# Kernel tuning notes

Hardware: AMD Instinct MI355X
Metric: run time of the kernel (lower is better)

## Reference

```python
import jax, jax.numpy as jnp
import numpy as np

HEADS = 8
DIM_HEAD = 32
EPS = 1e-5


def _rel_index(h, w):
    # matches Attention._generate_relative_index (static, computed on host)
    coords = np.stack(np.meshgrid(np.arange(h), np.arange(w), indexing='ij')).reshape(2, -1)
    rel = coords[:, :, None] - coords[:, None, :]  # [2, n, n]
    rel[0] += h - 1
    rel[1] += w - 1
    rel[0] *= 2 * w - 1
    idx = rel.sum(0).reshape(-1)
    # torch.clamp(relative_index, 0, max_index) -- indices are already in range here
    return jnp.asarray(np.clip(idx, 0, (2 * h - 1) * (2 * w - 1) - 1))


def _layernorm(x, g, b):
    m = jnp.mean(x, axis=-1, keepdims=True)
    v = jnp.var(x, axis=-1, keepdims=True)
    return (x - m) * jax.lax.rsqrt(v + EPS) * g + b


def setup_inputs() -> dict:
    key = jax.random.key(0)
    ks = jax.random.split(key, 6)
    B, C, H, W = 64, 384, 16, 16
    inner = HEADS * DIM_HEAD  # 256
    hid = 4 * C               # 1536
    def nrm(k, shape, s=0.02):
        return jax.random.normal(k, shape, jnp.float32) * s
    return {
        'x': jax.random.normal(ks[0], (B, C, H, W), jnp.float32),
        'ln1_g': jnp.ones((C,), jnp.float32),
        'ln1_b': jnp.zeros((C,), jnp.float32),
        'w_qkv': nrm(ks[1], (C, 3 * inner)),
        'bias_table': nrm(ks[2], ((2 * H - 1) * (2 * W - 1), HEADS)),
        'w_out': nrm(ks[3], (inner, C)),
        'b_out': jnp.zeros((C,), jnp.float32),
        'ln2_g': jnp.ones((C,), jnp.float32),
        'ln2_b': jnp.zeros((C,), jnp.float32),
        'w_ff1': nrm(ks[4], (C, hid)),
        'b_ff1': jnp.zeros((hid,), jnp.float32),
        'w_ff2': nrm(ks[5], (hid, C)),
        'b_ff2': jnp.zeros((C,), jnp.float32),
    }


def reference(x, ln1_g, ln1_b, w_qkv, bias_table, w_out, b_out,
              ln2_g, ln2_b, w_ff1, b_ff1, w_ff2, b_ff2):
    B, C, H, W = x.shape
    n = H * W
    t = x.reshape(B, C, n).transpose(0, 2, 1)  # [B, n, C]

    # --- attention branch (PreNorm(LayerNorm) -> Attention) ---
    a = _layernorm(t, ln1_g, ln1_b)
    qkv = a @ w_qkv  # [B, n, 3*inner]
    q, k, v = jnp.split(qkv, 3, axis=-1)
    def split_heads(z):
        return z.reshape(B, n, HEADS, DIM_HEAD).transpose(0, 2, 1, 3)  # [B, h, n, d]
    q, k, v = split_heads(q), split_heads(k), split_heads(v)
    dots = jnp.einsum('bhid,bhjd->bhij', q, k) * (DIM_HEAD ** -0.5)
    idx = _rel_index(H, W)  # [n*n]
    rel_bias = bias_table[idx].reshape(n, n, HEADS).transpose(2, 0, 1)[None]  # [1, h, n, n]
    attn = jax.nn.softmax(dots + rel_bias, axis=-1)
    o = jnp.einsum('bhij,bhjd->bhid', attn, v)
    o = o.transpose(0, 2, 1, 3).reshape(B, n, HEADS * DIM_HEAD)
    attn_out = o @ w_out + b_out  # to_out Linear (dropout=0)

    # --- feedforward branch (PreNorm(LayerNorm) -> FFN) ---
    f = _layernorm(t, ln2_g, ln2_b)
    f = jax.nn.gelu(f @ w_ff1 + b_ff1, approximate=False) @ w_ff2 + b_ff2

    y = t + attn_out + f  # x_adjusted + attn_out + ff_out
    return y.transpose(0, 2, 1).reshape(B, C, H, W)
```

## Files before the change

### kernel.cpp

```cpp
#include <hip/hip_runtime.h>

typedef __bf16 bf16;
typedef __bf16 bf16x8 __attribute__((ext_vector_type(8)));
typedef float f32x4 __attribute__((ext_vector_type(4)));

__device__ __forceinline__ void gll16(const void* g, void* l) {
    __builtin_amdgcn_global_load_lds((const __attribute__((address_space(1))) void*)g,
                                     (__attribute__((address_space(3))) void*)l, 16, 0, 0);
}

__device__ __forceinline__ float gelu_f(float v) {
    float x2 = v * v;
    float sn = v * fmaf(-0.0713540072f, x2, -1.5957691216f);
    float e  = __expf(sn);
    return v * __builtin_amdgcn_rcpf(1.0f + e);
}

__launch_bounds__(256)
__global__ void prep_kernel(const float* __restrict__ wqkv, const float* __restrict__ wout,
                            const float* __restrict__ wff1, const float* __restrict__ wff2,
                            bf16* __restrict__ wqkvT, bf16* __restrict__ woutT,
                            bf16* __restrict__ wff1T, bf16* __restrict__ wff2T,
                            const float* __restrict__ x,
                            const float* __restrict__ g1, const float* __restrict__ b1,
                            const float* __restrict__ g2, const float* __restrict__ b2,
                            bf16* __restrict__ a, bf16* __restrict__ f) {
    __shared__ __align__(16) float smem[12672 + 512 + 64];
    const int tid = threadIdx.x;
    int g = blockIdx.x;
    if (g < 1536) {
        float (*tl)[33] = (float (*)[33])smem;
        const float* in; bf16* out; int R, Cc, bx, by;
        if (g < 288)       { in = wqkv; out = wqkvT; R = 384;  Cc = 768;  bx = g % 24; by = g / 24; }
        else if (g < 384)  { g -= 288; in = wout; out = woutT; R = 256;  Cc = 384;  bx = g % 12; by = g / 12; }
        else if (g < 960)  { g -= 384; in = wff1; out = wff1T; R = 384;  Cc = 1536; bx = g % 48; by = g / 48; }
        else               { g -= 960; in = wff2; out = wff2T; R = 1536; Cc = 384;  bx = g % 12; by = g / 12; }
        const int c0 = bx * 32, r0 = by * 32;
        const int cl = tid & 31, r8 = tid >> 5;
#pragma unroll
        for (int k = 0; k < 4; k++) {
            int r = k * 8 + r8;
            tl[r][cl] = in[(size_t)(r0 + r) * Cc + c0 + cl];
        }
        __syncthreads();
#pragma unroll
        for (int k = 0; k < 4; k++) {
            int cc = k * 8 + r8;
            out[(size_t)(c0 + cc) * R + r0 + cl] = (bf16)tl[cl][cc];
        }
        return;
    }
    g -= 1536;
    float (*tile)[33] = (float (*)[33])smem;
    float (*S)[32]  = (float (*)[32])(smem + 12672);
    float (*SS)[32] = (float (*)[32])(smem + 12928);
    float* Mn = smem + 13184;
    float* Rs = smem + 13216;
    const int bb = g >> 3;
    const int i0 = (g & 7) * 32;
    {
        const int i_l = tid & 31, c_l = tid >> 5;
        const size_t base = (size_t)bb * 384 * 256 + i0 + i_l;
#pragma unroll 6
        for (int c = c_l; c < 384; c += 8)
            tile[c][i_l] = x[base + (size_t)c * 256];
    }
    __syncthreads();
    {
        const int i_s = tid & 31, p = tid >> 5;
        float s = 0.f, ss = 0.f;
#pragma unroll 6
        for (int j = 0; j < 48; j++) {
            float v = tile[p * 48 + j][i_s];
            s += v; ss += v * v;
        }
        S[p][i_s] = s; SS[p][i_s] = ss;
    }
    __syncthreads();
    if (tid < 32) {
        float t1 = 0.f, t2 = 0.f;
#pragma unroll
        for (int p = 0; p < 8; p++) { t1 += S[p][tid]; t2 += SS[p][tid]; }
        float mean = t1 * (1.0f / 384.0f);
        float var  = t2 * (1.0f / 384.0f) - mean * mean;
        Mn[tid] = mean;
        Rs[tid] = rsqrtf(var + 1e-5f);
    }
    __syncthreads();
    const int lane = tid & 63, w = tid >> 6;
#pragma unroll
    for (int rr = 0; rr < 8; rr++) {
        const int i = w * 8 + rr;
        const float mean = Mn[i], rstd = Rs[i];
        const size_t orow = ((size_t)bb * 256 + i0 + i) * 384;
#pragma unroll
        for (int pass = 0; pass < 6; pass++) {
            const int c = pass * 64 + lane;
            float nh = (tile[c][i] - mean) * rstd;
            a[orow + c] = (bf16)(nh * g1[c] + b1[c]);
            f[orow + c] = (bf16)(nh * g2[c] + b2[c]);
        }
    }
}

template <int EPI>
__launch_bounds__(256)
__global__ void gemm_bt(const bf16* __restrict__ A, const bf16* __restrict__ Bt,
                        const float* __restrict__ bias, bf16* __restrict__ C,
                        int M, int N, int K, int nx) {
    __shared__ bf16 lds[16384];
    const int tid = threadIdx.x;
    const int g = blockIdx.x;
    const int x = (g >> 3) % nx;
    const int y = (g & 7) + 8 * (g / (8 * nx));
    const int m0 = y * 128, n0 = x * 128;
    const int lane = tid & 63, w = tid >> 6;
    const int l16 = lane & 15, quad = lane >> 4;
    const int wm = (w & 1) * 64, wn = (w >> 1) * 64;

    f32x4 zero = {0.f, 0.f, 0.f, 0.f};
    f32x4 acc[4][4];
#pragma unroll
    for (int i = 0; i < 4; i++)
#pragma unroll
        for (int j = 0; j < 4; j++) acc[i][j] = zero;

    const int c0 = tid, c1 = tid + 256;
    const int r0 = c0 >> 2, k0c = (c0 & 3) * 8;
    const int r1 = c1 >> 2, k1c = (c1 & 3) * 8;
    const bf16* Abase = A + (size_t)m0 * K;
    const bf16* Bbase = Bt + (size_t)n0 * K;

#define STAGE128(buf, kb)                                                   \
    {                                                                       \
        bf16* lA = lds + (buf) * 8192;                                      \
        bf16* lB = lA + 4096;                                               \
        gll16(Abase + (size_t)r0 * K + (kb) + k0c, lA + c0 * 8);            \
        gll16(Abase + (size_t)r1 * K + (kb) + k1c, lA + c1 * 8);            \
        gll16(Bbase + (size_t)r0 * K + (kb) + k0c, lB + c0 * 8);            \
        gll16(Bbase + (size_t)r1 * K + (kb) + k1c, lB + c1 * 8);            \
    }

    STAGE128(0, 0);
    __syncthreads();
    int cur = 0;
    for (int kb = 0; kb < K; kb += 32) {
        if (kb + 32 < K) STAGE128(cur ^ 1, kb + 32);
        const bf16* lA = lds + cur * 8192;
        const bf16* lB = lA + 4096;
        bf16x8 af[4], bfr[4];
#pragma unroll
        for (int i = 0; i < 4; i++)
            af[i] = *(const bf16x8*)(lA + (wm + i * 16 + l16) * 32 + quad * 8);
#pragma unroll
        for (int j = 0; j < 4; j++)
            bfr[j] = *(const bf16x8*)(lB + (wn + j * 16 + l16) * 32 + quad * 8);
#pragma unroll
        for (int i = 0; i < 4; i++)
#pragma unroll
            for (int j = 0; j < 4; j++)
                acc[i][j] = __builtin_amdgcn_mfma_f32_16x16x32_bf16(af[i], bfr[j], acc[i][j], 0, 0, 0);
        __syncthreads();
        cur ^= 1;
    }
#undef STAGE128

#pragma unroll
    for (int j = 0; j < 4; j++) {
        const int col = wn + j * 16 + l16;
        float bv = 0.f;
        if (EPI >= 1) bv = bias[n0 + col];
#pragma unroll
        for (int i = 0; i < 4; i++) {
            const int row0 = wm + i * 16 + quad * 4;
#pragma unroll
            for (int r = 0; r < 4; r++) {
                float v = acc[i][j][r] + bv;
                if (EPI == 2) v = gelu_f(v);
                lds[(row0 + r) * 128 + col] = (bf16)v;
            }
        }
    }
    __syncthreads();
#pragma unroll
    for (int it = 0; it < 8; it++) {
        const int ch = tid + it * 256;
        const int row = ch >> 4, cc = (ch & 15) * 8;
        *(bf16x8*)(C + (size_t)(m0 + row) * N + n0 + cc) = *(const bf16x8*)(lds + row * 128 + cc);
    }
}

#define GEMM64_PROLOGUE_AND_KLOOP                                                   \
    const int tid = threadIdx.x;                                                    \
    const int g = blockIdx.x;                                                       \
    const int x_ = (g >> 3) % nx;                                                   \
    const int y_ = (g & 7) + 8 * (g / (8 * nx));                                    \
    const int m0 = y_ * 128, n0 = x_ * 64;                                          \
    const int lane = tid & 63, w = tid >> 6;                                        \
    const int l16 = lane & 15, quad = lane >> 4;                                    \
    const int wm = (w & 1) * 64, wn = (w >> 1) * 32;                                \
    f32x4 zero = {0.f, 0.f, 0.f, 0.f};                                              \
    f32x4 acc[4][2];                                                                \
    _Pragma("unroll") for (int i = 0; i < 4; i++)                                   \
        _Pragma("unroll") for (int j = 0; j < 2; j++) acc[i][j] = zero;             \
    const int c0 = tid, c1 = tid + 256;                                             \
    const int r0 = c0 >> 2, k0c = (c0 & 3) * 8;                                     \
    const int r1 = c1 >> 2, k1c = (c1 & 3) * 8;                                     \
    const int rB = tid >> 2, kBc = (tid & 3) * 8;                                   \
    const bf16* Abase = A + (size_t)m0 * K;                                         \
    const bf16* Bbase = Bt + (size_t)n0 * K;                                        \
    STAGE64(0, 0);                                                                  \
    __syncthreads();                                                                \
    int cur = 0;                                                                    \
    for (int kb = 0; kb < K; kb += 32) {                                            \
        if (kb + 32 < K) STAGE64(cur ^ 1, kb + 32);                                 \
        const bf16* lA = lds + cur * 6144;                                          \
        const bf16* lB = lA + 4096;                                                 \
        bf16x8 af[4], bfr[2];                                                       \
        _Pragma("unroll") for (int i = 0; i < 4; i++)                               \
            af[i] = *(const bf16x8*)(lA + (wm + i * 16 + l16) * 32 + quad * 8);     \
        _Pragma("unroll") for (int j = 0; j < 2; j++)                               \
            bfr[j] = *(const bf16x8*)(lB + (wn + j * 16 + l16) * 32 + quad * 8);    \
        _Pragma("unroll") for (int i = 0; i < 4; i++)                               \
            _Pragma("unroll") for (int j = 0; j < 2; j++)                           \
                acc[i][j] = __builtin_amdgcn_mfma_f32_16x16x32_bf16(af[i], bfr[j], acc[i][j], 0, 0, 0); \
        __syncthreads();                                                            \
        cur ^= 1;                                                                   \
    }

#define STAGE64(buf, kb)                                                            \
    {                                                                               \
        bf16* lA = lds + (buf) * 6144;                                              \
        bf16* lB = lA + 4096;                                                       \
        gll16(Abase + (size_t)r0 * K + (kb) + k0c, lA + c0 * 8);                    \
        gll16(Abase + (size_t)r1 * K + (kb) + k1c, lA + c1 * 8);                    \
        gll16(Bbase + (size_t)rB * K + (kb) + kBc, lB + tid * 8);                   \
    }

__launch_bounds__(256)
__global__ void gemm_bt_tr64(const bf16* __restrict__ A, const bf16* __restrict__ Bt,
                             const float* __restrict__ bias, bf16* __restrict__ Ct,
                             int M, int N, int K, int nx) {
    __shared__ bf16 lds[12288];
    GEMM64_PROLOGUE_AND_KLOOP
#pragma unroll
    for (int j = 0; j < 2; j++) {
        const int col = wn + j * 16 + l16;
        const float bv = bias[n0 + col];
#pragma unroll
        for (int i = 0; i < 4; i++) {
            const int row0 = wm + i * 16 + quad * 4;
#pragma unroll
            for (int r = 0; r < 4; r++)
                lds[col * 132 + row0 + r] = (bf16)(acc[i][j][r] + bv);
        }
    }
    __syncthreads();
    const int b = m0 >> 8, ib = m0 & 255;
#pragma unroll
    for (int it = 0; it < 4; it++) {
        const int ch = tid + it * 256;
        const int cl = ch >> 4, ic = (ch & 15) * 8;
        *(bf16x8*)(Ct + ((size_t)(b * 384 + n0 + cl) * 256 + ib + ic)) =
            *(const bf16x8*)(lds + cl * 132 + ic);
    }
}

__launch_bounds__(256)
__global__ void gemm_bt_final64(const bf16* __restrict__ A, const bf16* __restrict__ Bt,
                                const float* __restrict__ bias,
                                const float* __restrict__ xres, const bf16* __restrict__ attn_t,
                                float* __restrict__ out, int M, int N, int K, int nx) {
    __shared__ bf16 lds[12288];
    GEMM64_PROLOGUE_AND_KLOOP
#pragma unroll
    for (int j = 0; j < 2; j++) {
        const int col = wn + j * 16 + l16;
        const float bv = bias[n0 + col];
#pragma unroll
        for (int i = 0; i < 4; i++) {
            const int row0 = wm + i * 16 + quad * 4;
#pragma unroll
            for (int r = 0; r < 4; r++)
                lds[col * 132 + row0 + r] = (bf16)(acc[i][j][r] + bv);
        }
    }
    __syncthreads();
    const int b = m0 >> 8, ib = m0 & 255;
#pragma unroll
    for (int it = 0; it < 4; it++) {
        const int ch = tid + it * 256;
        const int cl = ch >> 4, ic = (ch & 15) * 8;
        const size_t base = (size_t)(b * 384 + n0 + cl) * 256 + ib + ic;
        bf16x8 ff = *(const bf16x8*)(lds + cl * 132 + ic);
        bf16x8 at = *(const bf16x8*)(attn_t + base);
        const f32x4* xr = (const f32x4*)(xres + base);
        f32x4 o0, o1;
#pragma unroll
        for (int e = 0; e < 4; e++) o0[e] = xr[0][e] + (float)at[e] + (float)ff[e];
#pragma unroll
        for (int e = 0; e < 4; e++) o1[e] = xr[1][e] + (float)at[e + 4] + (float)ff[e + 4];
        ((f32x4*)(out + base))[0] = o0;
        ((f32x4*)(out + base))[1] = o1;
    }
}

__launch_bounds__(256)
__global__ void attn_kernel(const bf16* __restrict__ qkv,
                            const float* __restrict__ btab,
                            bf16* __restrict__ o) {
    __shared__ float sbias[961];
    __shared__ __align__(16) bf16 sK[256 * 32];
    __shared__ __align__(16) bf16 sVt[32][264];
    __shared__ __align__(16) bf16 sP[4][16][264];
    const int tid = threadIdx.x;
    const int g = blockIdx.x;
    const int h  = (g >> 3) & 7;
    const int bb = (g & 7) + 8 * (g >> 6);
    const int lane = tid & 63, w = tid >> 6;
    const int l16 = lane & 15, quad = lane >> 4;
    const size_t qkvb = (size_t)bb * 256 * 768;
    const bf16* Qbase = qkv + qkvb + h * 32;
    const bf16* Kbase = qkv + qkvb + 256 + h * 32;
    const bf16* Vbase = qkv + qkvb + 512 + h * 32;

    for (int e = tid; e < 961; e += 256) sbias[e] = btab[e * 8 + h];
#pragma unroll
    for (int it = 0; it < 4; it++) {
        const int ch = it * 256 + tid;
        const int row = ch >> 2, d8 = (ch & 3) * 8;
        gll16(Kbase + (size_t)row * 768 + d8, sK + ch * 8);
    }
#pragma unroll
    for (int it = 0; it < 4; it++) {
        const int ch = it * 256 + tid;
        const int k = ch >> 2, d8 = (ch & 3) * 8;
        bf16x8 vv = *(const bf16x8*)(Vbase + (size_t)k * 768 + d8);
#pragma unroll
        for (int j = 0; j < 8; j++)
            sVt[d8 + j][k] = vv[j];
    }
    __syncthreads();

    f32x4 zero = {0.f, 0.f, 0.f, 0.f};
    for (int qc = 0; qc < 4; qc++) {
        const int qbase = qc * 64 + w * 16;
        bf16x8 qf = *(const bf16x8*)(Qbase + (size_t)(qbase + l16) * 768 + quad * 8);
        f32x4 s[16];
#pragma unroll
        for (int kt = 0; kt < 16; kt++) {
            bf16x8 kf = *(const bf16x8*)(sK + (kt * 16 + l16) * 32 + quad * 8);
            s[kt] = __builtin_amdgcn_mfma_f32_16x16x32_bf16(qf, kf, zero, 0, 0, 0);
        }
        const int qi0 = qbase + quad * 4;
        float mx[4] = {-1e30f, -1e30f, -1e30f, -1e30f};
#pragma unroll
        for (int kt = 0; kt < 16; kt++) {
            const int j = kt * 16 + l16;
            const int yj = j >> 4, xj = j & 15;
#pragma unroll
            for (int r = 0; r < 4; r++) {
                const int q = qi0 + r;
                const int tix = ((q >> 4) - yj + 15) * 31 + ((q & 15) - xj + 15);
                float v = s[kt][r] * 0.17677669529663687f + sbias[tix];
                s[kt][r] = v;
                mx[r] = fmaxf(mx[r], v);
            }
        }
#pragma unroll
        for (int r = 0; r < 4; r++)
            for (int msk = 1; msk < 16; msk <<= 1)
                mx[r] = fmaxf(mx[r], __shfl_xor(mx[r], msk, 64));
        float sum[4] = {0.f, 0.f, 0.f, 0.f};
#pragma unroll
        for (int kt = 0; kt < 16; kt++)
#pragma unroll
            for (int r = 0; r < 4; r++) {
                float e = __expf(s[kt][r] - mx[r]);
                s[kt][r] = e;
                sum[r] += e;
            }
#pragma unroll
        for (int r = 0; r < 4; r++) {
            for (int msk = 1; msk < 16; msk <<= 1)
                sum[r] += __shfl_xor(sum[r], msk, 64);
            sum[r] = 1.0f / sum[r];
        }
#pragma unroll
        for (int kt = 0; kt < 16; kt++)
#pragma unroll
            for (int r = 0; r < 4; r++)
                sP[w][quad * 4 + r][kt * 16 + l16] = (bf16)(s[kt][r] * sum[r]);
        f32x4 oacc[2];
        oacc[0] = zero; oacc[1] = zero;
#pragma unroll
        for (int ks = 0; ks < 8; ks++) {
            bf16x8 pf = *(const bf16x8*)(&sP[w][l16][ks * 32 + quad * 8]);
#pragma unroll
            for (int dt = 0; dt < 2; dt++) {
                bf16x8 vf = *(const bf16x8*)(&sVt[dt * 16 + l16][ks * 32 + quad * 8]);
                oacc[dt] = __builtin_amdgcn_mfma_f32_16x16x32_bf16(pf, vf, oacc[dt], 0, 0, 0);
            }
        }
#pragma unroll
        for (int dt = 0; dt < 2; dt++)
#pragma unroll
            for (int r = 0; r < 4; r++)
                o[(size_t)(bb * 256 + qbase + quad * 4 + r) * 256 + h * 32 + dt * 16 + l16] = (bf16)oacc[dt][r];
    }
}

extern "C" void kernel_launch(void* const* d_in, const int* in_sizes, int n_in,
                              void* d_out, int out_size, void* d_ws, size_t ws_size,
                              hipStream_t stream) {
    const float* x    = (const float*)d_in[0];
    const float* g1   = (const float*)d_in[1];
    const float* b1   = (const float*)d_in[2];
    const float* wqkv = (const float*)d_in[3];
    const float* btab = (const float*)d_in[4];
    const float* wout = (const float*)d_in[5];
    const float* bout = (const float*)d_in[6];
    const float* g2   = (const float*)d_in[7];
    const float* b2   = (const float*)d_in[8];
    const float* wff1 = (const float*)d_in[9];
    const float* bff1 = (const float*)d_in[10];
    const float* wff2 = (const float*)d_in[11];
    const float* bff2 = (const float*)d_in[12];
    float* out = (float*)d_out;

    bf16* ws = (bf16*)d_ws;
    const size_t NA = 6291456;
    bf16* wqkvT = ws;
    bf16* woutT = wqkvT + 294912;
    bf16* wff1T = woutT + 98304;
    bf16* wff2T = wff1T + 589824;
    bf16* f_buf    = ws + 1572864;
    bf16* attn_t   = f_buf + NA;
    bf16* R        = attn_t + NA;
    bf16* a_buf    = R;
    bf16* qkv_buf  = R + NA;
    bf16* o_buf    = R;
    bf16* ffh_buf  = R;

    dim3 b256(256);
    prep_kernel<<<2048, b256, 0, stream>>>(wqkv, wout, wff1, wff2, wqkvT, woutT, wff1T, wff2T,
                                           x, g1, b1, g2, b2, a_buf, f_buf);

    gemm_bt<0><<<6 * 128, b256, 0, stream>>>(a_buf, wqkvT, nullptr, qkv_buf, 16384, 768, 384, 6);
    attn_kernel<<<512, b256, 0, stream>>>(qkv_buf, btab, o_buf);
    gemm_bt_tr64<<<6 * 128, b256, 0, stream>>>(o_buf, woutT, bout, attn_t, 16384, 384, 256, 6);
    gemm_bt<2><<<12 * 128, b256, 0, stream>>>(f_buf, wff1T, bff1, ffh_buf, 16384, 1536, 384, 12);
    gemm_bt_final64<<<6 * 128, b256, 0, stream>>>(ffh_buf, wff2T, bff2, x, attn_t, out,
                                                  16384, 384, 1536, 6);
}
```

Measured before the change: 229.7 us.

## Deepen GEMM k-loop pipelines with multi-buffered LDS and vmcnt-based barriers

```diff
diff --git a/kernel.cpp b/kernel.cpp
--- a/kernel.cpp
+++ b/kernel.cpp
@@ -8,6 +8,8 @@
     __builtin_amdgcn_global_load_lds((const __attribute__((address_space(1))) void*)g,
                                      (__attribute__((address_space(3))) void*)l, 16, 0, 0);
 }
+
+#define WBAR(N) asm volatile("s_waitcnt vmcnt(" #N ")\n\ts_barrier" ::: "memory")
 
 __device__ __forceinline__ float gelu_f(float v) {
     float x2 = v * v;
@@ -108,7 +110,7 @@
 __global__ void gemm_bt(const bf16* __restrict__ A, const bf16* __restrict__ Bt,
                         const float* __restrict__ bias, bf16* __restrict__ C,
                         int M, int N, int K, int nx) {
-    __shared__ bf16 lds[16384];
+    __shared__ __align__(16) bf16 lds[24576];
     const int tid = threadIdx.x;
     const int g = blockIdx.x;
     const int x = (g >> 3) % nx;
@@ -133,37 +135,41 @@
 
 #define STAGE128(buf, kb)                                                   \
     {                                                                       \
-        bf16* lA = lds + (buf) * 8192;                                      \
-        bf16* lB = lA + 4096;                                               \
-        gll16(Abase + (size_t)r0 * K + (kb) + k0c, lA + c0 * 8);            \
-        gll16(Abase + (size_t)r1 * K + (kb) + k1c, lA + c1 * 8);            \
-        gll16(Bbase + (size_t)r0 * K + (kb) + k0c, lB + c0 * 8);            \
-        gll16(Bbase + (size_t)r1 * K + (kb) + k1c, lB + c1 * 8);            \
+        bf16* sA = lds + (buf) * 8192;                                      \
+        bf16* sB = sA + 4096;                                               \
+        gll16(Abase + (size_t)r0 * K + (kb) + k0c, sA + c0 * 8);            \
+        gll16(Abase + (size_t)r1 * K + (kb) + k1c, sA + c1 * 8);            \
+        gll16(Bbase + (size_t)r0 * K + (kb) + k0c, sB + c0 * 8);            \
+        gll16(Bbase + (size_t)r1 * K + (kb) + k1c, sB + c1 * 8);            \
+    }
+#define COMPUTE128(buf)                                                     \
+    {                                                                       \
+        const bf16* sA = lds + (buf) * 8192;                                \
+        const bf16* sB = sA + 4096;                                         \
+        bf16x8 af[4], bfr[4];                                               \
+        _Pragma("unroll") for (int i = 0; i < 4; i++)                       \
+            af[i] = *(const bf16x8*)(sA + (wm + i * 16 + l16) * 32 + quad * 8); \
+        _Pragma("unroll") for (int j = 0; j < 4; j++)                       \
+            bfr[j] = *(const bf16x8*)(sB + (wn + j * 16 + l16) * 32 + quad * 8); \
+        _Pragma("unroll") for (int i = 0; i < 4; i++)                       \
+            _Pragma("unroll") for (int j = 0; j < 4; j++)                   \
+                acc[i][j] = __builtin_amdgcn_mfma_f32_16x16x32_bf16(af[i], bfr[j], acc[i][j], 0, 0, 0); \
     }
 
     STAGE128(0, 0);
-    __syncthreads();
-    int cur = 0;
-    for (int kb = 0; kb < K; kb += 32) {
-        if (kb + 32 < K) STAGE128(cur ^ 1, kb + 32);
-        const bf16* lA = lds + cur * 8192;
-        const bf16* lB = lA + 4096;
-        bf16x8 af[4], bfr[4];
-#pragma unroll
-        for (int i = 0; i < 4; i++)
-            af[i] = *(const bf16x8*)(lA + (wm + i * 16 + l16) * 32 + quad * 8);
-#pragma unroll
-        for (int j = 0; j < 4; j++)
-            bfr[j] = *(const bf16x8*)(lB + (wn + j * 16 + l16) * 32 + quad * 8);
-#pragma unroll
-        for (int i = 0; i < 4; i++)
-#pragma unroll
-            for (int j = 0; j < 4; j++)
-                acc[i][j] = __builtin_amdgcn_mfma_f32_16x16x32_bf16(af[i], bfr[j], acc[i][j], 0, 0, 0);
-        __syncthreads();
-        cur ^= 1;
-    }
+    STAGE128(1, 32);
+    const int nt = K >> 5;
+    int t = 0;
+    for (; t < nt - 2; ++t) {
+        WBAR(4);
+        STAGE128((t + 2) % 3, (t + 2) * 32);
+        COMPUTE128(t % 3);
+    }
+    WBAR(4); COMPUTE128(t % 3); ++t;
+    WBAR(0); COMPUTE128(t % 3);
+    __syncthreads();
 #undef STAGE128
+#undef COMPUTE128
 
 #pragma unroll
     for (int j = 0; j < 4; j++) {
@@ -189,6 +195,28 @@
         *(bf16x8*)(C + (size_t)(m0 + row) * N + n0 + cc) = *(const bf16x8*)(lds + row * 128 + cc);
     }
 }
+
+#define STAGE64(buf, kb)                                                            \
+    {                                                                               \
+        bf16* sA = lds + (buf) * 6144;                                              \
+        bf16* sB = sA + 4096;                                                       \
+        gll16(Abase + (size_t)r0 * K + (kb) + k0c, sA + c0 * 8);                    \
+        gll16(Abase + (size_t)r1 * K + (kb) + k1c, sA + c1 * 8);                    \
+        gll16(Bbase + (size_t)rB * K + (kb) + kBc, sB + tid * 8);                   \
+    }
+#define COMPUTE64(buf)                                                              \
+    {                                                                               \
+        const bf16* sA = lds + (buf) * 6144;                                        \
+        const bf16* sB = sA + 4096;                                                 \
+        bf16x8 af[4], bfr[2];                                                       \
+        _Pragma("unroll") for (int i = 0; i < 4; i++)                               \
+            af[i] = *(const bf16x8*)(sA + (wm + i * 16 + l16) * 32 + quad * 8);     \
+        _Pragma("unroll") for (int j = 0; j < 2; j++)                               \
+            bfr[j] = *(const bf16x8*)(sB + (wn + j * 16 + l16) * 32 + quad * 8);    \
+        _Pragma("unroll") for (int i = 0; i < 4; i++)                               \
+            _Pragma("unroll") for (int j = 0; j < 2; j++)                           \
+                acc[i][j] = __builtin_amdgcn_mfma_f32_16x16x32_bf16(af[i], bfr[j], acc[i][j], 0, 0, 0); \
+    }
 
 #define GEMM64_PROLOGUE_AND_KLOOP                                                   \
     const int tid = threadIdx.x;                                                    \
@@ -209,39 +237,24 @@
     const int rB = tid >> 2, kBc = (tid & 3) * 8;                                   \
     const bf16* Abase = A + (size_t)m0 * K;                                         \
     const bf16* Bbase = Bt + (size_t)n0 * K;                                        \
-    STAGE64(0, 0);                                                                  \
-    __syncthreads();                                                                \
-    int cur = 0;                                                                    \
-    for (int kb = 0; kb < K; kb += 32) {                                            \
-        if (kb + 32 < K) STAGE64(cur ^ 1, kb + 32);                                 \
-        const bf16* lA = lds + cur * 6144;                                          \
-        const bf16* lB = lA + 4096;                                                 \
-        bf16x8 af[4], bfr[2];                                                       \
-        _Pragma("unroll") for (int i = 0; i < 4; i++)                               \
-            af[i] = *(const bf16x8*)(lA + (wm + i * 16 + l16) * 32 + quad * 8);     \
-        _Pragma("unroll") for (int j = 0; j < 2; j++)                               \
-            bfr[j] = *(const bf16x8*)(lB + (wn + j * 16 + l16) * 32 + quad * 8);    \
-        _Pragma("unroll") for (int i = 0; i < 4; i++)                               \
-            _Pragma("unroll") for (int j = 0; j < 2; j++)                           \
-                acc[i][j] = __builtin_amdgcn_mfma_f32_16x16x32_bf16(af[i], bfr[j], acc[i][j], 0, 0, 0); \
-        __syncthreads();                                                            \
-        cur ^= 1;                                                                   \
-    }
-
-#define STAGE64(buf, kb)                                                            \
-    {                                                                               \
-        bf16* lA = lds + (buf) * 6144;                                              \
-        bf16* lB = lA + 4096;                                                       \
-        gll16(Abase + (size_t)r0 * K + (kb) + k0c, lA + c0 * 8);                    \
-        gll16(Abase + (size_t)r1 * K + (kb) + k1c, lA + c1 * 8);                    \
-        gll16(Bbase + (size_t)rB * K + (kb) + kBc, lB + tid * 8);                   \
-    }
+    STAGE64(0, 0); STAGE64(1, 32); STAGE64(2, 64);                                  \
+    const int nt = K >> 5;                                                          \
+    int t = 0;                                                                      \
+    for (; t < nt - 3; ++t) {                                                       \
+        WBAR(6);                                                                    \
+        STAGE64((t + 3) & 3, (t + 3) * 32);                                         \
+        COMPUTE64(t & 3);                                                           \
+    }                                                                               \
+    WBAR(6); COMPUTE64(t & 3); ++t;                                                 \
+    WBAR(3); COMPUTE64(t & 3); ++t;                                                 \
+    WBAR(0); COMPUTE64(t & 3);                                                      \
+    __syncthreads();
 
 __launch_bounds__(256)
 __global__ void gemm_bt_tr64(const bf16* __restrict__ A, const bf16* __restrict__ Bt,
                              const float* __restrict__ bias, bf16* __restrict__ Ct,
                              int M, int N, int K, int nx) {
-    __shared__ bf16 lds[12288];
+    __shared__ __align__(16) bf16 lds[24576];
     GEMM64_PROLOGUE_AND_KLOOP
 #pragma unroll
     for (int j = 0; j < 2; j++) {
@@ -271,7 +284,7 @@
                                 const float* __restrict__ bias,
                                 const float* __restrict__ xres, const bf16* __restrict__ attn_t,
                                 float* __restrict__ out, int M, int N, int K, int nx) {
-    __shared__ bf16 lds[12288];
+    __shared__ __align__(16) bf16 lds[24576];
     GEMM64_PROLOGUE_AND_KLOOP
 #pragma unroll
     for (int j = 0; j < 2; j++) {
```

After: 229.3 us. About the same (-0.2%).
